# Optimization experiments

Measured on AMD Instinct MI355X. Metric: run time of the kernel, lower is better.

## Reference

```python
import jax, jax.numpy as jnp
import numpy as np

B, C, IC, H, W = 16, 256, 128, 32, 32  # batch, in_channels, inter_channels, spatial
EPS = 1e-5


def _conv1x1(x, w, b=None):
    # x: [B,C,H,W], w: [O,C] -> [B,O,H,W]
    y = jnp.einsum('bchw,oc->bohw', x, w)
    if b is not None:
        y = y + b[None, :, None, None]
    return y


def _dot_kernel(x, wt, wp):
    # relu-matmul attention, symmetrized, degree-rsqrt normalized with zero masking
    b, _, h, w = x.shape
    n = h * w
    t = jnp.maximum(_conv1x1(x, wt), 0.0).reshape(b, -1, n)  # [B,IC,N]
    p = jnp.maximum(_conv1x1(x, wp), 0.0).reshape(b, -1, n)  # [B,IC,N]
    att = jnp.einsum('bcn,bcm->bnm', t, p)                    # [B,N,N]
    att = (att + att.transpose(0, 2, 1)) * 0.5
    d = att.sum(axis=2)                                       # [B,N]
    dinv = jnp.where(d != 0, jax.lax.rsqrt(jnp.where(d != 0, d, 1.0)), 0.0)
    return att * dinv[:, None, :] * dinv[:, :, None]


def _bn(x, gamma, beta):
    # BatchNorm2d in training mode (batch statistics, biased variance)
    mu = jnp.mean(x, axis=(0, 2, 3), keepdims=True)
    var = jnp.mean((x - mu) ** 2, axis=(0, 2, 3), keepdims=True)
    xhat = (x - mu) * jax.lax.rsqrt(var + EPS)
    return xhat * gamma[None, :, None, None] + beta[None, :, None, None]


def setup_inputs() -> dict:
    key = jax.random.key(0)
    ks = jax.random.split(key, 32)
    s = 0.05
    inp = {
        'x':  jax.random.normal(ks[0], (B, C, H, W), jnp.float32),
        'ob': jax.random.normal(ks[1], (B, C, H, W), jnp.float32),
        'od': jax.random.normal(ks[2], (B, C, H, W), jnp.float32),
        'Wt': jax.random.normal(ks[3], (IC, C), jnp.float32) * s,
        'Wp': jax.random.normal(ks[4], (IC, C), jnp.float32) * s,
        'Wgx': jax.random.normal(ks[5], (IC, C), jnp.float32) * s,
        'bgx': jax.random.normal(ks[6], (IC,), jnp.float32) * s,
        'Wgb': jax.random.normal(ks[7], (IC, C), jnp.float32) * s,
        'bgb': jax.random.normal(ks[8], (IC,), jnp.float32) * s,
        'Wgd': jax.random.normal(ks[9], (IC, C), jnp.float32) * s,
        'bgd': jax.random.normal(ks[10], (IC,), jnp.float32) * s,
        'Wwx': jax.random.normal(ks[11], (C, IC), jnp.float32) * s,
        'bwx': jax.random.normal(ks[12], (C,), jnp.float32) * s,
        'Wwb': jax.random.normal(ks[13], (C, IC), jnp.float32) * s,
        'bwb': jax.random.normal(ks[14], (C,), jnp.float32) * s,
        'Wwd': jax.random.normal(ks[15], (C, IC), jnp.float32) * s,
        'bwd': jax.random.normal(ks[16], (C,), jnp.float32) * s,
        'Wwxb': jax.random.normal(ks[17], (C, IC), jnp.float32) * s,
        'bwxb': jax.random.normal(ks[18], (C,), jnp.float32) * s,
        'Wwxd': jax.random.normal(ks[19], (C, IC), jnp.float32) * s,
        'bwxd': jax.random.normal(ks[20], (C,), jnp.float32) * s,
        'gamma1': jnp.ones((C,), jnp.float32),
        'beta1': jnp.zeros((C,), jnp.float32),
        'gamma2': jnp.ones((C,), jnp.float32),
        'beta2': jnp.zeros((C,), jnp.float32),
        'Wout': jax.random.normal(ks[21], (C, C), jnp.float32) * s,
        'bout': jax.random.normal(ks[22], (C,), jnp.float32) * s,
    }
    return inp


def reference(x, ob, od, Wt, Wp, Wgx, bgx, Wgb, bgb, Wgd, bgd,
              Wwx, bwx, Wwb, bwb, Wwd, bwd, Wwxb, bwxb, Wwxd, bwxd,
              gamma1, beta1, gamma2, beta2, Wout, bout):
    b, c, h, w = x.shape
    n = h * w

    def g_tokens(inp, wg, bg):
        return _conv1x1(inp, wg, bg).reshape(b, -1, n).transpose(0, 2, 1)  # [B,N,IC]

    g_x = g_tokens(x, Wgx, bgx)
    g_b = g_tokens(ob, Wgb, bgb)
    g_d = g_tokens(od, Wgd, bgd)

    f_x = _dot_kernel(x, Wt, Wp)
    f_b = _dot_kernel(ob, Wt, Wp)
    f_d = _dot_kernel(od, Wt, Wp)

    def agg(f, g):
        # bmm(f,g).transpose(1,2).view(B,IC,H,W)
        return jnp.einsum('bnm,bmi->bin', f, g).reshape(b, -1, h, w)

    x_self = _conv1x1(agg(f_x, g_x), Wwx, bwx)
    ob_self = _conv1x1(agg(f_b, g_b), Wwb, bwb)
    od_self = _conv1x1(agg(f_d, g_d), Wwd, bwd)
    x_ob_cross = _conv1x1(agg(f_b, g_x), Wwxb, bwxb)
    x_od_cross = _conv1x1(agg(f_d, g_x), Wwxd, bwxd)

    od_final = _bn(od_self + x_ob_cross, gamma1, beta1)
    ob_final = _bn(ob_self + x_od_cross, gamma2, beta2)
    output = _conv1x1(od_final + ob_final + x_self, Wout, bout)
    return output + x
```

## Files before the change

kernel.cpp:

```cpp
#include <hip/hip_runtime.h>

#define GAS __attribute__((address_space(1)))
#define LAS __attribute__((address_space(3)))

typedef __attribute__((ext_vector_type(8))) short short8;
typedef __attribute__((ext_vector_type(4))) float f32x4;
typedef unsigned short u16;

constexpr int cB = 16, cC = 256, cIC = 128, cN = 1024;

__device__ __forceinline__ u16 f2bf(float v) {
    unsigned u = __builtin_bit_cast(unsigned, v);
    return (u16)((u + 0x7fffu + ((u >> 16) & 1u)) >> 16);
}
__device__ __forceinline__ float bf2f(u16 v) {
    unsigned u = ((unsigned)v) << 16;
    return __builtin_bit_cast(float, u);
}
__device__ __forceinline__ float rsz(float d) {
    return (d != 0.0f) ? rsqrtf(d) : 0.0f;
}

template<int N> __device__ __forceinline__ void wait_vmcnt() {
    if constexpr (N == 0) asm volatile("s_waitcnt vmcnt(0)" ::: "memory");
    else if constexpr (N == 1) asm volatile("s_waitcnt vmcnt(1)" ::: "memory");
    else if constexpr (N == 2) asm volatile("s_waitcnt vmcnt(2)" ::: "memory");
    else if constexpr (N == 3) asm volatile("s_waitcnt vmcnt(3)" ::: "memory");
    else if constexpr (N == 4) asm volatile("s_waitcnt vmcnt(4)" ::: "memory");
    else if constexpr (N == 5) asm volatile("s_waitcnt vmcnt(5)" ::: "memory");
    else if constexpr (N == 6) asm volatile("s_waitcnt vmcnt(6)" ::: "memory");
}

template<int BM, int BN, int WR, int WC, bool BREMAP = false>
__device__ __forceinline__ void gemm_core(
    const u16* __restrict__ Ab, const u16* __restrict__ Ab2, int ksplit, int lda,
    const u16* __restrict__ Bb, int ldb, int K,
    u16* lsA, u16* lsB,
    f32x4 (&acc)[BM/(WR*16)][BN/(WC*16)])
{
    constexpr int THREADS = WR * WC * 64;
    constexpr int MR = BM / (WR * 16), NR = BN / (WC * 16);
    constexpr int ACH = (BM * 64) / (THREADS * 16);
    constexpr int BCH = (BN * 64) / (THREADS * 16);
    constexpr int RPC = THREADS / 4;
    constexpr int ISSUES = ACH + BCH;

    const int tid  = threadIdx.x;
    const int lane = tid & 63;
    const int wave = tid >> 6;
    const int wr = wave / WC, wc = wave % WC;
    const int r0 = tid >> 2, slot = tid & 3;

    auto stage = [&](int buf, int kk) {
        const u16* Ak = (Ab2 != nullptr && kk >= ksplit) ? (Ab2 + (kk - ksplit)) : (Ab + kk);
        const u16* Bk = Bb + (BREMAP ? (((kk >> 7) << 8) + (kk & 127)) : kk);
        #pragma unroll
        for (int c = 0; c < ACH; c++) {
            int row = c * RPC + r0;
            int sk = (slot ^ ((row >> 1) & 3)) << 3;
            __builtin_amdgcn_global_load_lds((GAS void*)(Ak + (size_t)row * lda + sk),
                (LAS void*)(lsA + buf * (BM * 32) + c * (THREADS * 8) + (wave << 9)), 16, 0, 0);
        }
        #pragma unroll
        for (int c = 0; c < BCH; c++) {
            int row = c * RPC + r0;
            int sk = (slot ^ ((row >> 1) & 3)) << 3;
            __builtin_amdgcn_global_load_lds((GAS void*)(Bk + (size_t)row * ldb + sk),
                (LAS void*)(lsB + buf * (BN * 32) + c * (THREADS * 8) + (wave << 9)), 16, 0, 0);
        }
    };

    stage(0, 0);
    const int nt = K >> 5;
    for (int t = 0; t < nt; t++) {
        const int cur = t & 1;
        if (t + 1 < nt) { stage(cur ^ 1, (t + 1) << 5); wait_vmcnt<ISSUES>(); }
        else            wait_vmcnt<0>();
        __builtin_amdgcn_s_barrier();
        asm volatile("" ::: "memory");

        const u16* la = lsA + cur * (BM * 32);
        const u16* lb = lsB + cur * (BN * 32);
        short8 af[MR], bf[NR];
        #pragma unroll
        for (int m = 0; m < MR; m++) {
            int row = wr * (BM / WR) + (m << 4) + (lane & 15);
            af[m] = *(const short8*)&la[(row << 5) + (((lane >> 4) ^ ((row >> 1) & 3)) << 3)];
        }
        #pragma unroll
        for (int n = 0; n < NR; n++) {
            int row = wc * (BN / WC) + (n << 4) + (lane & 15);
            bf[n] = *(const short8*)&lb[(row << 5) + (((lane >> 4) ^ ((row >> 1) & 3)) << 3)];
        }
        #pragma unroll
        for (int m = 0; m < MR; m++)
            #pragma unroll
            for (int n = 0; n < NR; n++)
                acc[m][n] = __builtin_amdgcn_mfma_f32_16x16x32_bf16(af[m], bf[n], acc[m][n], 0, 0, 0);

        asm volatile("s_waitcnt lgkmcnt(0)" ::: "memory");
        __builtin_amdgcn_sched_barrier(0);
        __builtin_amdgcn_s_barrier();
    }
}

template<int BM, int BN, int WR, int WC, bool RELU, bool OBF16, bool RBIAS, bool RESID>
__global__ __launch_bounds__(WR*WC*64) void gemm_bt(
    const u16* __restrict__ A, long long sA, long long sA2, int lda,
    const u16* __restrict__ B, long long sB, long long sB2, int ldb,
    void* __restrict__ C, long long sC, long long sC2, int ldc,
    int K,
    const float* __restrict__ bias, int sb2,
    const float* __restrict__ resid, long long sR)
{
    __shared__ alignas(16) u16 lsA[2 * BM * 32];
    __shared__ alignas(16) u16 lsB[2 * BN * 32];

    const int lane = threadIdx.x & 63;
    const int wave = threadIdx.x >> 6;
    const int wr = wave / WC, wc = wave % WC;
    const int zlo = blockIdx.z & 15, zhi = blockIdx.z >> 4;

    const u16* Ab = A + zlo * sA + zhi * sA2 + (size_t)(blockIdx.x * BM) * lda;
    const u16* Bb = B + zlo * sB + zhi * sB2 + (size_t)(blockIdx.y * BN) * ldb;

    f32x4 acc[BM/(WR*16)][BN/(WC*16)] = {};
    gemm_core<BM, BN, WR, WC>(Ab, nullptr, K, lda, Bb, ldb, K, lsA, lsB, acc);

    const int rowb = blockIdx.x * BM + wr * (BM / WR) + ((lane >> 4) << 2);
    const int colb = blockIdx.y * BN + wc * (BN / WC) + (lane & 15);
    const long long cbase = zlo * sC + zhi * sC2;
    #pragma unroll
    for (int m = 0; m < BM/(WR*16); m++) {
        #pragma unroll
        for (int n = 0; n < BN/(WC*16); n++) {
            #pragma unroll
            for (int r = 0; r < 4; r++) {
                int row = rowb + m * 16 + r;
                int col = colb + n * 16;
                float v = acc[m][n][r];
                if (RBIAS) v += bias[zhi * sb2 + row];
                if (RESID) v += resid[zlo * sR + (size_t)row * ldc + col];
                if (RELU)  v = fmaxf(v, 0.0f);
                if (OBF16) ((u16*)C)[cbase + (size_t)row * ldc + col] = f2bf(v);
                else       ((float*)C)[cbase + (size_t)row * ldc + col] = v;
            }
        }
    }
}

__global__ __launch_bounds__(512) void tp_gemm(
    const u16* __restrict__ XT, const u16* __restrict__ WTP,
    u16* __restrict__ TPt, u16* __restrict__ TP, float* __restrict__ CS)
{
    __shared__ alignas(16) u16 lsA[2 * 128 * 32];
    __shared__ alignas(16) u16 lsB[2 * 256 * 32];

    const int id = blockIdx.x;
    const int lane = threadIdx.x & 63;
    const int wave = threadIdx.x >> 6;
    const int wr = wave >> 2, wc = wave & 3;

    if (id < 384) {
        const int z = id >> 3, r_ = id & 7, cx = r_ >> 2, ny = r_ & 3;
        const u16* Ab = WTP + (size_t)(cx * 128) * 256;
        const u16* Bb = XT + (size_t)z * 262144 + (size_t)(ny * 256) * 256;
        f32x4 acc[4][4] = {};
        gemm_core<128, 256, 2, 4>(Ab, nullptr, 256, 256, Bb, 256, 256, lsA, lsB, acc);

        const int rowb = cx * 128 + wr * 64 + ((lane >> 4) << 2);
        const int colb = ny * 256 + wc * 64 + (lane & 15);
        u16* Cb = TPt + (size_t)z * 262144;
        float rp[4][4] = {};
        #pragma unroll
        for (int m = 0; m < 4; m++)
            #pragma unroll
            for (int n = 0; n < 4; n++)
                #pragma unroll
                for (int r = 0; r < 4; r++) {
                    float v = fmaxf(acc[m][n][r], 0.0f);
                    Cb[(size_t)(rowb + m * 16 + r) * 1024 + colb + n * 16] = f2bf(v);
                    rp[m][r] += v;
                }
        #pragma unroll
        for (int m = 0; m < 4; m++)
            #pragma unroll
            for (int r = 0; r < 4; r++) {
                float v = rp[m][r];
                v += __shfl_xor(v, 1, 64);
                v += __shfl_xor(v, 2, 64);
                v += __shfl_xor(v, 4, 64);
                v += __shfl_xor(v, 8, 64);
                if ((lane & 15) == 0)
                    atomicAdd(&CS[z * 256 + rowb + m * 16 + r], v);
            }
    } else {
        const int id2 = id - 384;
        const int z = id2 >> 3, nx = id2 & 7;
        const u16* Ab = XT + (size_t)z * 262144 + (size_t)(nx * 128) * 256;
        f32x4 acc[4][4] = {};
        gemm_core<128, 256, 2, 4>(Ab, nullptr, 256, 256, WTP, 256, 256, lsA, lsB, acc);

        const int rowb = nx * 128 + wr * 64 + ((lane >> 4) << 2);
        const int colb = wc * 64 + (lane & 15);
        u16* Cb = TP + (size_t)z * 262144;
        #pragma unroll
        for (int m = 0; m < 4; m++)
            #pragma unroll
            for (int n = 0; n < 4; n++)
                #pragma unroll
                for (int r = 0; r < 4; r++)
                    Cb[(size_t)(rowb + m * 16 + r) * 256 + colb + n * 16] =
                        f2bf(fmaxf(acc[m][n][r], 0.0f));
    }
}

__global__ __launch_bounds__(256) void dinv_mv(
    const u16* __restrict__ TPt, const float* __restrict__ CS, float* __restrict__ DINV)
{
    const int z = blockIdx.y;
    const int n = blockIdx.x * 256 + threadIdx.x;
    __shared__ float ws[256];
    ws[threadIdx.x] = 0.5f * CS[z * 256 + (threadIdx.x ^ 128)];
    __syncthreads();
    const u16* base = TPt + (size_t)z * 262144 + n;
    float d = 0;
    #pragma unroll 8
    for (int c = 0; c < 256; c++) d += bf2f(base[(size_t)c << 10]) * ws[c];
    DINV[(z << 10) + n] = d;
}

__global__ __launch_bounds__(256) void g_gemm(
    const u16* __restrict__ XT, const u16* __restrict__ WG,
    const float* __restrict__ BG, const float* __restrict__ DINV,
    u16* __restrict__ GXp, u16* __restrict__ GBp, u16* __restrict__ GDp)
{
    __shared__ alignas(16) u16 lsA[2 * 128 * 32];
    __shared__ alignas(16) u16 lsB[2 * 128 * 32];

    const int yb = blockIdx.x, zs = blockIdx.z;
    const int stream = zs >> 4, b = zs & 15;

    const u16* Ab = WG + stream * 32768;
    const u16* Bb = XT + (size_t)zs * 262144 + (size_t)(yb * 128) * 256;

    f32x4 acc[4][4] = {};
    gemm_core<128, 128, 2, 2>(Ab, nullptr, 256, 256, Bb, 256, 256, lsA, lsB, acc);

    const int lane = threadIdx.x & 63;
    const int wave = threadIdx.x >> 6;
    const int wr = wave >> 1, wc = wave & 1;
    const int rowb = (wr << 6) + ((lane >> 4) << 2);
    const int colb = yb * 128 + (wc << 6) + (lane & 15);
    const float* dvx = DINV + (b << 10);
    const float* dvb = DINV + 16384 + (b << 10);
    const float* dvd = DINV + 32768 + (b << 10);
    float sx[4], sb_[4], sd[4];
    #pragma unroll
    for (int n = 0; n < 4; n++) {
        int col = colb + n * 16;
        if (stream == 0) { sx[n] = rsz(dvx[col]); sb_[n] = rsz(dvb[col]); sd[n] = rsz(dvd[col]); }
        else if (stream == 1) sb_[n] = rsz(dvb[col]);
        else sd[n] = rsz(dvd[col]);
    }
    #pragma unroll
    for (int m = 0; m < 4; m++) {
        #pragma unroll
        for (int r = 0; r < 4; r++) {
            int row = rowb + m * 16 + r;
            float bias = BG[stream * 128 + row];
            #pragma unroll
            for (int n = 0; n < 4; n++) {
                int col = colb + n * 16;
                float v = acc[m][n][r] + bias;
                if (stream == 0) {
                    GXp[(size_t)b * 131072 + ((size_t)row << 10) + col] = f2bf(v * sx[n]);
                    GBp[(size_t)b * 262144 + ((size_t)(row + 128) << 10) + col] = f2bf(v * sb_[n]);
                    GDp[(size_t)b * 262144 + ((size_t)(row + 128) << 10) + col] = f2bf(v * sd[n]);
                } else if (stream == 1) {
                    GBp[(size_t)b * 262144 + ((size_t)row << 10) + col] = f2bf(v * sb_[n]);
                } else {
                    GDp[(size_t)b * 262144 + ((size_t)row << 10) + col] = f2bf(v * sd[n]);
                }
            }
        }
    }
}

__global__ __launch_bounds__(256) void inner_splitk(
    const u16* __restrict__ TPt, const u16* __restrict__ GXp,
    const u16* __restrict__ GBp, const u16* __restrict__ GDp,
    u16* __restrict__ MX, u16* __restrict__ MB, u16* __restrict__ MD)
{
    __shared__ alignas(16) u16 lsA[2 * 128 * 32];
    __shared__ alignas(16) u16 lsB[2 * 128 * 32];

    const int bz = blockIdx.z;
    const int split = bz / 48, z = bz % 48;
    const int which = z >> 4, b = z & 15;
    if (which == 0 && blockIdx.y) return;
    const u16* Gp = (which == 0) ? GXp : (which == 1) ? GBp : GDp;
    u16* M = (which == 0) ? MX : (which == 1) ? MB : MD;
    const int JD  = (which == 0) ? 128 : 256;
    const int ldc = 2 * JD;
    const long long sB = (which == 0) ? 131072 : 262144;

    const u16* Ab = TPt + (size_t)z * 262144 + (size_t)(blockIdx.x * 128) * 1024 + split * 512;
    const u16* Bb = Gp + (size_t)b * sB + (size_t)(blockIdx.y * 128) * 1024 + split * 512;

    f32x4 acc[4][4] = {};
    gemm_core<128, 128, 2, 2>(Ab, nullptr, 512, 1024, Bb, 1024, 512, lsA, lsB, acc);

    const int lane = threadIdx.x & 63;
    const int wave = threadIdx.x >> 6;
    const int wr = wave >> 1, wc = wave & 1;
    const int rowb = blockIdx.x * 128 + (wr << 6) + ((lane >> 4) << 2);
    const int colb = blockIdx.y * 128 + (wc << 6) + (lane & 15);
    u16* Cb = M + (size_t)b * (256 * ldc);
    #pragma unroll
    for (int m = 0; m < 4; m++)
        #pragma unroll
        for (int n = 0; n < 4; n++)
            #pragma unroll
            for (int r = 0; r < 4; r++) {
                int row = (rowb + m * 16 + r) ^ 128;
                int col = split * JD + colb + n * 16;
                Cb[(size_t)row * ldc + col] = f2bf(acc[m][n][r]);
            }
}

__global__ __launch_bounds__(512) void fold_gemm(
    const u16* __restrict__ WF2, const u16* __restrict__ MX,
    const u16* __restrict__ MB, const u16* __restrict__ MD,
    u16* __restrict__ FF2)
{
    __shared__ alignas(16) u16 lsA[2 * 128 * 32];
    __shared__ alignas(16) u16 lsB[2 * 256 * 32];

    const int z = blockIdx.z, q = z >> 4, b = z & 15;
    const int pr = (q == 4) ? 2 : (q >> 1);
    const int side = (q == 1 || q == 3) ? 1 : 0;

    const u16* Ab = WF2 + q * 65536 + (size_t)(blockIdx.x * 128) * 256;

    f32x4 acc[4][4] = {};
    if (q == 4) {
        const u16* Bb = MX + (size_t)b * 65536;
        gemm_core<128, 256, 2, 4, false>(Ab, nullptr, 256, 256, Bb, 256, 256, lsA, lsB, acc);
    } else {
        const u16* Mp = (q == 1 || q == 2) ? MB : MD;
        const int coff = side ? 128 : 0;
        const u16* Bb = Mp + (size_t)b * 131072 + coff;
        gemm_core<128, 256, 2, 4, true>(Ab, nullptr, 256, 256, Bb, 512, 256, lsA, lsB, acc);
    }

    const int lane = threadIdx.x & 63;
    const int wave = threadIdx.x >> 6;
    const int wr = wave >> 2, wc = wave & 3;
    const int rowb = blockIdx.x * 128 + wr * 64 + ((lane >> 4) << 2);
    const int colb = wc * 64 + (lane & 15);
    u16* Cb = FF2 + (size_t)pr * 2097152 + (size_t)b * 131072;
    #pragma unroll
    for (int m = 0; m < 4; m++)
        #pragma unroll
        for (int n = 0; n < 4; n++)
            #pragma unroll
            for (int r = 0; r < 4; r++)
                Cb[(size_t)(rowb + m * 16 + r) * 512 + side * 256 + colb + n * 16]
                    = f2bf(acc[m][n][r]);
}

__global__ __launch_bounds__(512) void outer_gemm(
    const u16* __restrict__ TP, const u16* __restrict__ FF2,
    const float* __restrict__ DINV,
    u16* __restrict__ SALL, float* __restrict__ BNA)
{
    __shared__ alignas(16) u16 lsA[2 * 128 * 32];
    __shared__ alignas(16) u16 lsB[2 * 256 * 32];

    const int z = blockIdx.z, zhi = z >> 4, b = z & 15;
    const int sa1[3] = {2, 1, 0}, sa2[3] = {1, 2, 0};

    const int lane = threadIdx.x & 63;
    const int wave = threadIdx.x >> 6;
    const int wr = wave >> 2, wc = wave & 3;
    const int rowb = blockIdx.x * 128 + wr * 64 + ((lane >> 4) << 2);
    const int colb = wc * 64 + (lane & 15);

    const u16* A1 = TP + (size_t)(sa1[zhi] * 16 + b) * 262144 + (size_t)(blockIdx.x * 128) * 256;
    const u16* B1 = FF2 + (size_t)zhi * 2097152 + (size_t)b * 131072;
    const float* dv1 = DINV + sa1[zhi] * 16384 + (b << 10);

    f32x4 acc[4][4] = {};
    gemm_core<128, 256, 2, 4>(A1, nullptr, 256, 256, B1, 512, 256, lsA, lsB, acc);

    f32x4 keep[4][4];
    #pragma unroll
    for (int m = 0; m < 4; m++) {
        f32x4 dva;
        #pragma unroll
        for (int r = 0; r < 4; r++) dva[r] = rsz(dv1[rowb + m * 16 + r]);
        #pragma unroll
        for (int n = 0; n < 4; n++) keep[m][n] = acc[m][n] * dva;
    }

    if (zhi < 2) {
        const u16* A2 = TP + (size_t)(sa2[zhi] * 16 + b) * 262144 + (size_t)(blockIdx.x * 128) * 256;
        const u16* B2 = B1 + 256;
        const float* dv2 = DINV + sa2[zhi] * 16384 + (b << 10);
        #pragma unroll
        for (int m = 0; m < 4; m++)
            #pragma unroll
            for (int n = 0; n < 4; n++) acc[m][n] = f32x4{0.f, 0.f, 0.f, 0.f};
        gemm_core<128, 256, 2, 4>(A2, nullptr, 256, 256, B2, 512, 256, lsA, lsB, acc);
        #pragma unroll
        for (int m = 0; m < 4; m++) {
            f32x4 dva;
            #pragma unroll
            for (int r = 0; r < 4; r++) dva[r] = rsz(dv2[rowb + m * 16 + r]);
            #pragma unroll
            for (int n = 0; n < 4; n++) keep[m][n] = keep[m][n] + acc[m][n] * dva;
        }
    }

    u16* Cb = SALL + (size_t)b * 786432;
    float csum[4] = {}, csq[4] = {};
    #pragma unroll
    for (int m = 0; m < 4; m++)
        #pragma unroll
        for (int n = 0; n < 4; n++)
            #pragma unroll
            for (int r = 0; r < 4; r++) {
                float v = keep[m][n][r];
                Cb[(size_t)(rowb + m * 16 + r) * 768 + zhi * 256 + colb + n * 16] = f2bf(v);
                csum[n] += v;
                csq[n] += v * v;
            }
    if (zhi < 2) {
        #pragma unroll
        for (int n = 0; n < 4; n++) {
            float s = csum[n], q = csq[n];
            s += __shfl_xor(s, 16, 64); s += __shfl_xor(s, 32, 64);
            q += __shfl_xor(q, 16, 64); q += __shfl_xor(q, 32, 64);
            if (lane < 16) {
                atomicAdd(&BNA[zhi * 512 + colb + n * 16], s);
                atomicAdd(&BNA[zhi * 512 + 256 + colb + n * 16], q);
            }
        }
    }
}

__global__ __launch_bounds__(256) void bnscale(
    const float* __restrict__ Wout, const float* __restrict__ g1, const float* __restrict__ be1,
    const float* __restrict__ g2, const float* __restrict__ be2,
    const float* __restrict__ bwx, const float* __restrict__ bout,
    const float* __restrict__ BNA, u16* __restrict__ WoutS, float* __restrict__ BIAS2)
{
    int o = blockIdx.x, c = threadIdx.x;
    const float inv = 1.0f / 16384.0f;
    float m1 = BNA[c] * inv;
    float v1 = BNA[256 + c] * inv - m1 * m1;
    float sc1 = g1[c] * rsqrtf(v1 + 1e-5f), sh1 = be1[c] - m1 * sc1;
    float m2 = BNA[512 + c] * inv;
    float v2 = BNA[768 + c] * inv - m2 * m2;
    float sc2 = g2[c] * rsqrtf(v2 + 1e-5f), sh2 = be2[c] - m2 * sc2;
    float wv = Wout[o * 256 + c];
    WoutS[o * 768 + c]       = f2bf(wv * sc1);
    WoutS[o * 768 + 256 + c] = f2bf(wv * sc2);
    WoutS[o * 768 + 512 + c] = f2bf(wv);
    __shared__ float red[256];
    red[c] = wv * (sh1 + sh2 + bwx[c]);
    __syncthreads();
    for (int s = 128; s; s >>= 1) { if (c < s) red[c] += red[c + s]; __syncthreads(); }
    if (c == 0) BIAS2[o] = red[0] + bout[o];
}

__global__ void prep_transpose(const float* __restrict__ x, const float* __restrict__ ob,
                               const float* __restrict__ od, u16* __restrict__ xt,
                               const float* Wt, const float* Wp,
                               const float* Wgx, const float* Wgb, const float* Wgd,
                               const float* bgx, const float* bgb, const float* bgd,
                               const float* Wwd, const float* Wwxb, const float* Wwb,
                               const float* Wwxd, const float* Wwx,
                               u16* wtp, u16* wg, u16* wf2, float* bg,
                               float* __restrict__ ZZ)
{
    int tx = threadIdx.x, ty = threadIdx.y;
    if (blockIdx.z == 48) {
        int t = (blockIdx.y * 32 + blockIdx.x) * 256 + ty * 32 + tx;
        wtp[t] = f2bf(t < 32768 ? Wt[t] : Wp[t - 32768]);
        if (t < 32768) {
            wg[t] = f2bf(Wgx[t]); wg[32768 + t] = f2bf(Wgb[t]); wg[65536 + t] = f2bf(Wgd[t]);
        }
        {
            int o = t >> 8, k = t & 255, j = k & 127;
            const float* Wq[5] = {Wwd, Wwxb, Wwb, Wwxd, Wwx};
            #pragma unroll
            for (int q = 0; q < 5; q++)
                wf2[q * 65536 + t] = f2bf(0.5f * Wq[q][o * 128 + j]);
        }
        if (t < 384) bg[t] = (t < 128) ? bgx[t] : (t < 256) ? bgb[t - 128] : bgd[t - 256];
        if (t < 13312) ZZ[t] = 0.0f;
        return;
    }
    __shared__ float tbuf[32][33];
    int z = blockIdx.z, which = z >> 4, b = z & 15;
    const float* src = (which == 0) ? x : (which == 1) ? ob : od;
    const float* s = src + (size_t)b * cC * cN;
    u16* dst = xt + (size_t)which * (cB * cN * cC) + (size_t)b * (cN * cC);
    int n0 = blockIdx.x << 5, c0 = blockIdx.y << 5;
    #pragma unroll
    for (int i = 0; i < 4; i++) { int r = ty + (i << 3); tbuf[r][tx] = s[(size_t)(c0 + r) * cN + n0 + tx]; }
    __syncthreads();
    #pragma unroll
    for (int i = 0; i < 4; i++) { int r = ty + (i << 3); dst[(size_t)(n0 + r) * cC + c0 + tx] = f2bf(tbuf[tx][r]); }
}

extern "C" void kernel_launch(void* const* d_in, const int* in_sizes, int n_in,
                              void* d_out, int out_size, void* d_ws, size_t ws_size,
                              hipStream_t stream)
{
    const float* x    = (const float*)d_in[0];
    const float* ob   = (const float*)d_in[1];
    const float* od   = (const float*)d_in[2];
    const float* Wt   = (const float*)d_in[3];
    const float* Wp   = (const float*)d_in[4];
    const float* Wgx  = (const float*)d_in[5];
    const float* bgx  = (const float*)d_in[6];
    const float* Wgb  = (const float*)d_in[7];
    const float* bgb  = (const float*)d_in[8];
    const float* Wgd  = (const float*)d_in[9];
    const float* bgd  = (const float*)d_in[10];
    const float* Wwx  = (const float*)d_in[11];
    const float* bwx  = (const float*)d_in[12];
    const float* Wwb  = (const float*)d_in[13];
    const float* Wwd  = (const float*)d_in[15];
    const float* Wwxb = (const float*)d_in[17];
    const float* Wwxd = (const float*)d_in[19];
    const float* g1   = (const float*)d_in[21];
    const float* be1  = (const float*)d_in[22];
    const float* g2   = (const float*)d_in[23];
    const float* be2  = (const float*)d_in[24];
    const float* Wout = (const float*)d_in[25];
    const float* bout = (const float*)d_in[26];
    float* out = (float*)d_out;

    char* w = (char*)d_ws;
    u16*   XT    = (u16*)(w);
    u16*   TPt   = (u16*)(w + 25165824);
    u16*   TP    = (u16*)(w + 50331648);
    u16*   GXp   = (u16*)(w + 75497472);
    u16*   GBp   = (u16*)(w + 79691776);
    u16*   GDp   = (u16*)(w + 88080384);
    u16*   MX    = (u16*)(w + 96468992);
    u16*   MB    = (u16*)(w + 98566144);
    u16*   MD    = (u16*)(w + 102760448);
    u16*   FF2   = (u16*)(w + 106954752);
    u16*   WTP   = (u16*)(w + 119537664);
    u16*   WG    = (u16*)(w + 119668736);
    u16*   WF2   = (u16*)(w + 119865344);
    u16*   WoutS = (u16*)(w + 120520704);
    float* BGf   = (float*)(w + 120913920);
    float* BIAS2 = (float*)(w + 120915968);
    float* DINV  = (float*)(w + 120920064);
    float* ZZ    = (float*)(w + 121116672);

    float* CS   = ZZ;
    float* BNA  = ZZ + 12288;
    u16*   SALL = TPt;

    prep_transpose<<<dim3(32, 8, 49), dim3(32, 8), 0, stream>>>(
        x, ob, od, XT, Wt, Wp, Wgx, Wgb, Wgd, bgx, bgb, bgd,
        Wwd, Wwxb, Wwb, Wwxd, Wwx, WTP, WG, WF2, BGf, ZZ);

    tp_gemm<<<dim3(768), 512, 0, stream>>>(XT, WTP, TPt, TP, CS);

    dinv_mv<<<dim3(4, 48), 256, 0, stream>>>(TPt, CS, DINV);

    g_gemm<<<dim3(8, 1, 48), 256, 0, stream>>>(XT, WG, BGf, DINV, GXp, GBp, GDp);

    inner_splitk<<<dim3(2, 2, 96), 256, 0, stream>>>(TPt, GXp, GBp, GDp, MX, MB, MD);

    fold_gemm<<<dim3(2, 1, 80), 512, 0, stream>>>(WF2, MX, MB, MD, FF2);

    outer_gemm<<<dim3(8, 1, 48), 512, 0, stream>>>(TP, FF2, DINV, SALL, BNA);

    bnscale<<<dim3(256), 256, 0, stream>>>(Wout, g1, be1, g2, be2, bwx, bout,
                                           BNA, WoutS, BIAS2);

    gemm_bt<128, 128, 2, 2, false, false, true, true><<<dim3(2, 8, 16), 256, 0, stream>>>(
        WoutS, 0, 0, 768,  SALL, 786432, 0, 768,  out, 262144, 0, 1024,
        768, BIAS2, 0, x, 262144);
}
```

Before: 167.3 us.

## Shrink GEMM tiles to 128x128, remap blocks, vectorize prep transpose

tp_gemm and outer_gemm move from 128x256 tiles with 512 threads to 128x128 tiles with 256 threads. This doubles the block count so more blocks are in flight across the CUs. outer_gemm and the final projection now use a block-index swizzle that interleaves work across groups of blocks, likely to improve cache locality or XCD spread. The generic templated gemm_bt is replaced by a dedicated final_gemm, and prep_transpose uses 64x64 tiles with float4 loads and short8 stores instead of scalar 32x32 accesses. Smaller tiles mean less operand reuse per block and more atomics for the column sums.

```diff
diff --git a/kernel.cpp b/kernel.cpp
--- a/kernel.cpp
+++ b/kernel.cpp
@@ -29,6 +29,7 @@
     else if constexpr (N == 4) asm volatile("s_waitcnt vmcnt(4)" ::: "memory");
     else if constexpr (N == 5) asm volatile("s_waitcnt vmcnt(5)" ::: "memory");
     else if constexpr (N == 6) asm volatile("s_waitcnt vmcnt(6)" ::: "memory");
+    else if constexpr (N == 8) asm volatile("s_waitcnt vmcnt(8)" ::: "memory");
 }
 
 template<int BM, int BN, int WR, int WC, bool BREMAP = false>
@@ -104,72 +105,27 @@
     }
 }
 
-template<int BM, int BN, int WR, int WC, bool RELU, bool OBF16, bool RBIAS, bool RESID>
-__global__ __launch_bounds__(WR*WC*64) void gemm_bt(
-    const u16* __restrict__ A, long long sA, long long sA2, int lda,
-    const u16* __restrict__ B, long long sB, long long sB2, int ldb,
-    void* __restrict__ C, long long sC, long long sC2, int ldc,
-    int K,
-    const float* __restrict__ bias, int sb2,
-    const float* __restrict__ resid, long long sR)
-{
-    __shared__ alignas(16) u16 lsA[2 * BM * 32];
-    __shared__ alignas(16) u16 lsB[2 * BN * 32];
-
+__global__ __launch_bounds__(256) void tp_gemm(
+    const u16* __restrict__ XT, const u16* __restrict__ WTP,
+    u16* __restrict__ TPt, u16* __restrict__ TP, float* __restrict__ CS)
+{
+    __shared__ alignas(16) u16 lsA[2 * 128 * 32];
+    __shared__ alignas(16) u16 lsB[2 * 128 * 32];
+
+    const int id = blockIdx.x, z = blockIdx.z;
     const int lane = threadIdx.x & 63;
     const int wave = threadIdx.x >> 6;
-    const int wr = wave / WC, wc = wave % WC;
-    const int zlo = blockIdx.z & 15, zhi = blockIdx.z >> 4;
-
-    const u16* Ab = A + zlo * sA + zhi * sA2 + (size_t)(blockIdx.x * BM) * lda;
-    const u16* Bb = B + zlo * sB + zhi * sB2 + (size_t)(blockIdx.y * BN) * ldb;
-
-    f32x4 acc[BM/(WR*16)][BN/(WC*16)] = {};
-    gemm_core<BM, BN, WR, WC>(Ab, nullptr, K, lda, Bb, ldb, K, lsA, lsB, acc);
-
-    const int rowb = blockIdx.x * BM + wr * (BM / WR) + ((lane >> 4) << 2);
-    const int colb = blockIdx.y * BN + wc * (BN / WC) + (lane & 15);
-    const long long cbase = zlo * sC + zhi * sC2;
-    #pragma unroll
-    for (int m = 0; m < BM/(WR*16); m++) {
-        #pragma unroll
-        for (int n = 0; n < BN/(WC*16); n++) {
-            #pragma unroll
-            for (int r = 0; r < 4; r++) {
-                int row = rowb + m * 16 + r;
-                int col = colb + n * 16;
-                float v = acc[m][n][r];
-                if (RBIAS) v += bias[zhi * sb2 + row];
-                if (RESID) v += resid[zlo * sR + (size_t)row * ldc + col];
-                if (RELU)  v = fmaxf(v, 0.0f);
-                if (OBF16) ((u16*)C)[cbase + (size_t)row * ldc + col] = f2bf(v);
-                else       ((float*)C)[cbase + (size_t)row * ldc + col] = v;
-            }
-        }
-    }
-}
-
-__global__ __launch_bounds__(512) void tp_gemm(
-    const u16* __restrict__ XT, const u16* __restrict__ WTP,
-    u16* __restrict__ TPt, u16* __restrict__ TP, float* __restrict__ CS)
-{
-    __shared__ alignas(16) u16 lsA[2 * 128 * 32];
-    __shared__ alignas(16) u16 lsB[2 * 256 * 32];
-
-    const int id = blockIdx.x;
-    const int lane = threadIdx.x & 63;
-    const int wave = threadIdx.x >> 6;
-    const int wr = wave >> 2, wc = wave & 3;
-
-    if (id < 384) {
-        const int z = id >> 3, r_ = id & 7, cx = r_ >> 2, ny = r_ & 3;
+    const int wr = wave >> 1, wc = wave & 1;
+
+    if (id < 16) {
+        const int cx = id >> 3, ny = id & 7;
         const u16* Ab = WTP + (size_t)(cx * 128) * 256;
-        const u16* Bb = XT + (size_t)z * 262144 + (size_t)(ny * 256) * 256;
+        const u16* Bb = XT + (size_t)z * 262144 + (size_t)(ny * 128) * 256;
         f32x4 acc[4][4] = {};
-        gemm_core<128, 256, 2, 4>(Ab, nullptr, 256, 256, Bb, 256, 256, lsA, lsB, acc);
+        gemm_core<128, 128, 2, 2>(Ab, nullptr, 256, 256, Bb, 256, 256, lsA, lsB, acc);
 
         const int rowb = cx * 128 + wr * 64 + ((lane >> 4) << 2);
-        const int colb = ny * 256 + wc * 64 + (lane & 15);
+        const int colb = ny * 128 + wc * 64 + (lane & 15);
         u16* Cb = TPt + (size_t)z * 262144;
         float rp[4][4] = {};
         #pragma unroll
@@ -195,14 +151,15 @@
                     atomicAdd(&CS[z * 256 + rowb + m * 16 + r], v);
             }
     } else {
-        const int id2 = id - 384;
-        const int z = id2 >> 3, nx = id2 & 7;
+        const int id2 = id - 16;
+        const int nx = id2 >> 1, cy = id2 & 1;
         const u16* Ab = XT + (size_t)z * 262144 + (size_t)(nx * 128) * 256;
+        const u16* Bb = WTP + (size_t)(cy * 128) * 256;
         f32x4 acc[4][4] = {};
-        gemm_core<128, 256, 2, 4>(Ab, nullptr, 256, 256, WTP, 256, 256, lsA, lsB, acc);
+        gemm_core<128, 128, 2, 2>(Ab, nullptr, 256, 256, Bb, 256, 256, lsA, lsB, acc);
 
         const int rowb = nx * 128 + wr * 64 + ((lane >> 4) << 2);
-        const int colb = wc * 64 + (lane & 15);
+        const int colb = cy * 128 + wc * 64 + (lane & 15);
         u16* Cb = TP + (size_t)z * 262144;
         #pragma unroll
         for (int m = 0; m < 4; m++)
@@ -370,29 +327,31 @@
                     = f2bf(acc[m][n][r]);
 }
 
-__global__ __launch_bounds__(512) void outer_gemm(
+__global__ __launch_bounds__(256) void outer_gemm(
     const u16* __restrict__ TP, const u16* __restrict__ FF2,
     const float* __restrict__ DINV,
     u16* __restrict__ SALL, float* __restrict__ BNA)
 {
     __shared__ alignas(16) u16 lsA[2 * 128 * 32];
-    __shared__ alignas(16) u16 lsB[2 * 256 * 32];
-
-    const int z = blockIdx.z, zhi = z >> 4, b = z & 15;
+    __shared__ alignas(16) u16 lsB[2 * 128 * 32];
+
+    const int i = (blockIdx.x & 7) * 96 + (blockIdx.x >> 3);
+    const int z = i >> 4, r_ = i & 15, xb = r_ >> 1, ob = r_ & 1;
+    const int zhi = z >> 4, b = z & 15;
     const int sa1[3] = {2, 1, 0}, sa2[3] = {1, 2, 0};
 
     const int lane = threadIdx.x & 63;
     const int wave = threadIdx.x >> 6;
-    const int wr = wave >> 2, wc = wave & 3;
-    const int rowb = blockIdx.x * 128 + wr * 64 + ((lane >> 4) << 2);
-    const int colb = wc * 64 + (lane & 15);
-
-    const u16* A1 = TP + (size_t)(sa1[zhi] * 16 + b) * 262144 + (size_t)(blockIdx.x * 128) * 256;
-    const u16* B1 = FF2 + (size_t)zhi * 2097152 + (size_t)b * 131072;
+    const int wr = wave >> 1, wc = wave & 1;
+    const int rowb = xb * 128 + wr * 64 + ((lane >> 4) << 2);
+    const int colb = ob * 128 + wc * 64 + (lane & 15);
+
+    const u16* A1 = TP + (size_t)(sa1[zhi] * 16 + b) * 262144 + (size_t)(xb * 128) * 256;
+    const u16* B1 = FF2 + (size_t)zhi * 2097152 + (size_t)b * 131072 + (size_t)(ob * 128) * 512;
     const float* dv1 = DINV + sa1[zhi] * 16384 + (b << 10);
 
     f32x4 acc[4][4] = {};
-    gemm_core<128, 256, 2, 4>(A1, nullptr, 256, 256, B1, 512, 256, lsA, lsB, acc);
+    gemm_core<128, 128, 2, 2>(A1, nullptr, 256, 256, B1, 512, 256, lsA, lsB, acc);
 
     f32x4 keep[4][4];
     #pragma unroll
@@ -405,14 +364,14 @@
     }
 
     if (zhi < 2) {
-        const u16* A2 = TP + (size_t)(sa2[zhi] * 16 + b) * 262144 + (size_t)(blockIdx.x * 128) * 256;
+        const u16* A2 = TP + (size_t)(sa2[zhi] * 16 + b) * 262144 + (size_t)(xb * 128) * 256;
         const u16* B2 = B1 + 256;
         const float* dv2 = DINV + sa2[zhi] * 16384 + (b << 10);
         #pragma unroll
         for (int m = 0; m < 4; m++)
             #pragma unroll
             for (int n = 0; n < 4; n++) acc[m][n] = f32x4{0.f, 0.f, 0.f, 0.f};
-        gemm_core<128, 256, 2, 4>(A2, nullptr, 256, 256, B2, 512, 256, lsA, lsB, acc);
+        gemm_core<128, 128, 2, 2>(A2, nullptr, 256, 256, B2, 512, 256, lsA, lsB, acc);
         #pragma unroll
         for (int m = 0; m < 4; m++) {
             f32x4 dva;
@@ -448,6 +407,41 @@
             }
         }
     }
+}
+
+__global__ __launch_bounds__(256) void final_gemm(
+    const u16* __restrict__ WoutS, const u16* __restrict__ SALL,
+    const float* __restrict__ BIAS2, const float* __restrict__ x,
+    float* __restrict__ out)
+{
+    __shared__ alignas(16) u16 lsA[2 * 128 * 32];
+    __shared__ alignas(16) u16 lsB[2 * 128 * 32];
+
+    const int i = (blockIdx.x & 7) * 32 + (blockIdx.x >> 3);
+    const int b = i >> 4, r_ = i & 15, xb = r_ >> 3, yb = r_ & 7;
+
+    const u16* Ab = WoutS + (size_t)(xb * 128) * 768;
+    const u16* Bb = SALL + (size_t)b * 786432 + (size_t)(yb * 128) * 768;
+
+    f32x4 acc[4][4] = {};
+    gemm_core<128, 128, 2, 2>(Ab, nullptr, 768, 768, Bb, 768, 768, lsA, lsB, acc);
+
+    const int lane = threadIdx.x & 63;
+    const int wave = threadIdx.x >> 6;
+    const int wr = wave >> 1, wc = wave & 1;
+    const int rowb = xb * 128 + (wr << 6) + ((lane >> 4) << 2);
+    const int colb = yb * 128 + (wc << 6) + (lane & 15);
+    #pragma unroll
+    for (int m = 0; m < 4; m++)
+        #pragma unroll
+        for (int n = 0; n < 4; n++)
+            #pragma unroll
+            for (int r = 0; r < 4; r++) {
+                int row = rowb + m * 16 + r;
+                int col = colb + n * 16;
+                size_t idx = (size_t)b * 262144 + (size_t)row * 1024 + col;
+                out[idx] = acc[m][n][r] + BIAS2[row] + x[idx];
+            }
 }
 
 __global__ __launch_bounds__(256) void bnscale(
@@ -475,45 +469,63 @@
     if (c == 0) BIAS2[o] = red[0] + bout[o];
 }
 
-__global__ void prep_transpose(const float* __restrict__ x, const float* __restrict__ ob,
-                               const float* __restrict__ od, u16* __restrict__ xt,
-                               const float* Wt, const float* Wp,
-                               const float* Wgx, const float* Wgb, const float* Wgd,
-                               const float* bgx, const float* bgb, const float* bgd,
-                               const float* Wwd, const float* Wwxb, const float* Wwb,
-                               const float* Wwxd, const float* Wwx,
-                               u16* wtp, u16* wg, u16* wf2, float* bg,
-                               float* __restrict__ ZZ)
-{
-    int tx = threadIdx.x, ty = threadIdx.y;
+__global__ __launch_bounds__(256) void prep_transpose(
+    const float* __restrict__ x, const float* __restrict__ ob,
+    const float* __restrict__ od, u16* __restrict__ xt,
+    const float* Wt, const float* Wp,
+    const float* Wgx, const float* Wgb, const float* Wgd,
+    const float* bgx, const float* bgb, const float* bgd,
+    const float* Wwd, const float* Wwxb, const float* Wwb,
+    const float* Wwxd, const float* Wwx,
+    u16* wtp, u16* wg, u16* wf2, float* bg,
+    float* __restrict__ ZZ)
+{
+    const int tid = threadIdx.x;
     if (blockIdx.z == 48) {
-        int t = (blockIdx.y * 32 + blockIdx.x) * 256 + ty * 32 + tx;
-        wtp[t] = f2bf(t < 32768 ? Wt[t] : Wp[t - 32768]);
-        if (t < 32768) {
-            wg[t] = f2bf(Wgx[t]); wg[32768 + t] = f2bf(Wgb[t]); wg[65536 + t] = f2bf(Wgd[t]);
-        }
-        {
-            int o = t >> 8, k = t & 255, j = k & 127;
-            const float* Wq[5] = {Wwd, Wwxb, Wwb, Wwxd, Wwx};
-            #pragma unroll
-            for (int q = 0; q < 5; q++)
-                wf2[q * 65536 + t] = f2bf(0.5f * Wq[q][o * 128 + j]);
-        }
-        if (t < 384) bg[t] = (t < 128) ? bgx[t] : (t < 256) ? bgb[t - 128] : bgd[t - 256];
-        if (t < 13312) ZZ[t] = 0.0f;
+        int base = (blockIdx.y * 16 + blockIdx.x) * 1024;
+        #pragma unroll
+        for (int l = 0; l < 4; l++) {
+            int t = base + l * 256 + tid;
+            wtp[t] = f2bf(t < 32768 ? Wt[t] : Wp[t - 32768]);
+            if (t < 32768) {
+                wg[t] = f2bf(Wgx[t]); wg[32768 + t] = f2bf(Wgb[t]); wg[65536 + t] = f2bf(Wgd[t]);
+            }
+            {
+                int o = t >> 8, k = t & 255, j = k & 127;
+                const float* Wq[5] = {Wwd, Wwxb, Wwb, Wwxd, Wwx};
+                #pragma unroll
+                for (int q = 0; q < 5; q++)
+                    wf2[q * 65536 + t] = f2bf(0.5f * Wq[q][o * 128 + j]);
+            }
+            if (t < 384) bg[t] = (t < 128) ? bgx[t] : (t < 256) ? bgb[t - 128] : bgd[t - 256];
+            if (t < 13312) ZZ[t] = 0.0f;
+        }
         return;
     }
-    __shared__ float tbuf[32][33];
-    int z = blockIdx.z, which = z >> 4, b = z & 15;
+    __shared__ float ls[64][68];
+    const int z = blockIdx.z, which = z >> 4, b = z & 15;
     const float* src = (which == 0) ? x : (which == 1) ? ob : od;
     const float* s = src + (size_t)b * cC * cN;
-    u16* dst = xt + (size_t)which * (cB * cN * cC) + (size_t)b * (cN * cC);
-    int n0 = blockIdx.x << 5, c0 = blockIdx.y << 5;
-    #pragma unroll
-    for (int i = 0; i < 4; i++) { int r = ty + (i << 3); tbuf[r][tx] = s[(size_t)(c0 + r) * cN + n0 + tx]; }
+    u16* dst = xt + (size_t)z * (cN * cC);
+    const int n0 = blockIdx.x << 6, c0 = blockIdx.y << 6;
+
+    const int cl0 = tid >> 4, n4 = (tid & 15) << 2;
+    #pragma unroll
+    for (int p = 0; p < 4; p++) {
+        int cl = cl0 + (p << 4);
+        f32x4 v = *(const f32x4*)&s[(size_t)(c0 + cl) * cN + n0 + n4];
+        ls[cl][n4] = v[0]; ls[cl][n4 + 1] = v[1]; ls[cl][n4 + 2] = v[2]; ls[cl][n4 + 3] = v[3];
+    }
     __syncthreads();
-    #pragma unroll
-    for (int i = 0; i < 4; i++) { int r = ty + (i << 3); dst[(size_t)(n0 + r) * cC + c0 + tx] = f2bf(tbuf[tx][r]); }
+    const int nl0 = tid >> 3, c8 = (tid & 7) << 3;
+    #pragma unroll
+    for (int q = 0; q < 2; q++) {
+        int nl = nl0 + (q << 5);
+        short8 o;
+        #pragma unroll
+        for (int j = 0; j < 8; j++) o[j] = (short)f2bf(ls[c8 + j][nl]);
+        *(short8*)&dst[(size_t)(n0 + nl) * 256 + c0 + c8] = o;
+    }
 }
 
 extern "C" void kernel_launch(void* const* d_in, const int* in_sizes, int n_in,
@@ -569,11 +581,11 @@
     float* BNA  = ZZ + 12288;
     u16*   SALL = TPt;
 
-    prep_transpose<<<dim3(32, 8, 49), dim3(32, 8), 0, stream>>>(
+    prep_transpose<<<dim3(16, 4, 49), 256, 0, stream>>>(
         x, ob, od, XT, Wt, Wp, Wgx, Wgb, Wgd, bgx, bgb, bgd,
         Wwd, Wwxb, Wwb, Wwxd, Wwx, WTP, WG, WF2, BGf, ZZ);
 
-    tp_gemm<<<dim3(768), 512, 0, stream>>>(XT, WTP, TPt, TP, CS);
+    tp_gemm<<<dim3(32, 1, 48), 256, 0, stream>>>(XT, WTP, TPt, TP, CS);
 
     dinv_mv<<<dim3(4, 48), 256, 0, stream>>>(TPt, CS, DINV);
 
@@ -583,12 +595,10 @@
 
     fold_gemm<<<dim3(2, 1, 80), 512, 0, stream>>>(WF2, MX, MB, MD, FF2);
 
-    outer_gemm<<<dim3(8, 1, 48), 512, 0, stream>>>(TP, FF2, DINV, SALL, BNA);
+    outer_gemm<<<dim3(768), 256, 0, stream>>>(TP, FF2, DINV, SALL, BNA);
 
     bnscale<<<dim3(256), 256, 0, stream>>>(Wout, g1, be1, g2, be2, bwx, bout,
                                            BNA, WoutS, BIAS2);
 
-    gemm_bt<128, 128, 2, 2, false, false, true, true><<<dim3(2, 8, 16), 256, 0, stream>>>(
-        WoutS, 0, 0, 768,  SALL, 786432, 0, 768,  out, 262144, 0, 1024,
-        768, BIAS2, 0, x, 262144);
-}
+    final_gemm<<<dim3(256), 256, 0, stream>>>(WoutS, SALL, BIAS2, x, out);
+}
```

New measurement: 178.8 us. 6.9% more time.
